# Performance work log

Hardware: AMD Instinct MI355X
Metric: run time of the kernel (lower is better)

The kernel has to match this reference:

```python
import jax, jax.numpy as jnp
import numpy as np

T, H, NH, NKV, HD, E, K, I = 1024, 2048, 16, 4, 128, 16, 2, 768
EPS = 1e-6
THETA = 10000.0


def setup_inputs() -> dict:
    key = jax.random.key(0)
    ks = jax.random.split(key, 8)
    s = 0.02
    return {
        "hidden_states": jax.random.normal(ks[0], (T, H), jnp.float32),
        "positions": jnp.arange(T, dtype=jnp.int32),
        "w_norm1": jnp.ones((H,), jnp.float32),
        "w_norm2": jnp.ones((H,), jnp.float32),
        "w_qkv": jax.random.normal(ks[1], (H, (NH + 2 * NKV) * HD), jnp.float32) * s,
        "w_qnorm": jnp.ones((HD,), jnp.float32),
        "w_knorm": jnp.ones((HD,), jnp.float32),
        "w_o": jax.random.normal(ks[2], (NH * HD, H), jnp.float32) * s,
        "w_router": jax.random.normal(ks[3], (H, E), jnp.float32) * s,
        "w_gate": jax.random.normal(ks[4], (E, H, I), jnp.float32) * s,
        "w_up": jax.random.normal(ks[5], (E, H, I), jnp.float32) * s,
        "w_down": jax.random.normal(ks[6], (E, I, H), jnp.float32) * s,
    }


def rmsnorm(x, w):
    return x * jax.lax.rsqrt(jnp.mean(x * x, axis=-1, keepdims=True) + EPS) * w


def apply_rope(x, positions):
    # NEOX-style rotary, full head_dim. x: [T, n_heads, HD]
    half = HD // 2
    inv_freq = 1.0 / (THETA ** (jnp.arange(half, dtype=jnp.float32) / half))
    ang = positions.astype(jnp.float32)[:, None] * inv_freq  # [T, half]
    cos = jnp.cos(ang)[:, None, :]
    sin = jnp.sin(ang)[:, None, :]
    x1, x2 = x[..., :half], x[..., half:]
    return jnp.concatenate([x1 * cos - x2 * sin, x2 * cos + x1 * sin], axis=-1)


def reference(hidden_states, positions, w_norm1, w_norm2, w_qkv, w_qnorm, w_knorm,
              w_o, w_router, w_gate, w_up, w_down):
    # prepare_attn: residual = x; h = input_layernorm(x)
    residual = hidden_states
    h = rmsnorm(hidden_states, w_norm1)

    # --- attention (bidirectional, GQA, per-head q/k RMSNorm + RoPE) ---
    qkv = h @ w_qkv
    q, k, v = jnp.split(qkv, [NH * HD, NH * HD + NKV * HD], axis=-1)
    q = rmsnorm(q.reshape(T, NH, HD), w_qnorm)
    k = rmsnorm(k.reshape(T, NKV, HD), w_knorm)
    v = v.reshape(T, NKV, HD)
    q = apply_rope(q, positions)
    k = apply_rope(k, positions)
    rep = NH // NKV
    kf = jnp.repeat(k, rep, axis=1)  # [T, NH, HD]
    vf = jnp.repeat(v, rep, axis=1)
    scores = jnp.einsum('tnd,snd->nts', q, kf) * (HD ** -0.5)  # [NH, T, T]
    p = jax.nn.softmax(scores, axis=-1)
    ctx = jnp.einsum('nts,snd->tnd', p, vf).reshape(T, NH * HD)
    attn_out = ctx @ w_o

    # prepare_mlp: residual = residual + attn_out; h = post_attention_layernorm(residual)
    residual = residual + attn_out
    h = rmsnorm(residual, w_norm2)

    # --- sparse MoE: softmax router, top-k renormalize, SwiGLU experts ---
    logits = h @ w_router
    probs = jax.nn.softmax(logits, axis=-1)
    topw, topi = jax.lax.top_k(probs, K)
    topw = topw / jnp.sum(topw, axis=-1, keepdims=True)
    gates = jnp.zeros((T, E), h.dtype).at[jnp.arange(T)[:, None], topi].set(topw)
    g = jnp.einsum('th,ehi->eti', h, w_gate)
    u = jnp.einsum('th,ehi->eti', h, w_up)
    y = jnp.einsum('eti,eih->eth', jax.nn.silu(g) * u, w_down)
    moe_out = jnp.einsum('eth,te->th', y, gates)

    return moe_out, residual
```

## Files before the change

### kernel.cpp

```cpp
#include <hip/hip_runtime.h>

#define T_    1024
#define H_    2048
#define NH_   16
#define NKV_  4
#define HD_   128
#define E_    16
#define I_    768
#define QKVN  3072

typedef __attribute__((ext_vector_type(8))) short  short8;
typedef __attribute__((ext_vector_type(4))) float  f32x4;
typedef unsigned short u16;

#define LDPA 32
#define LDPB 40

__device__ inline u16 f2bf(float f) {
  unsigned u = __builtin_bit_cast(unsigned, f);
  return (u16)((u + 0x7fffu + ((u >> 16) & 1u)) >> 16);
}
__device__ inline float bf2f(u16 h) {
  unsigned u = ((unsigned)h) << 16;
  return __builtin_bit_cast(float, u);
}

__device__ inline void gll16(const u16* g, u16* l) {
  __builtin_amdgcn_global_load_lds(
      (const __attribute__((address_space(1))) void*)g,
      (__attribute__((address_space(3))) void*)l, 16, 0, 0);
}

__device__ inline float blk_sum(float v, float* lds) {
#pragma unroll
  for (int o = 32; o; o >>= 1) v += __shfl_down(v, o);
  int w = threadIdx.x >> 6;
  __syncthreads();
  if ((threadIdx.x & 63) == 0) lds[w] = v;
  __syncthreads();
  float s = lds[0];
  int nw = blockDim.x >> 6;
  for (int i = 1; i < nw; ++i) s += lds[i];
  return s;
}
__device__ inline float blk_max(float v, float* lds) {
#pragma unroll
  for (int o = 32; o; o >>= 1) v = fmaxf(v, __shfl_down(v, o));
  int w = threadIdx.x >> 6;
  __syncthreads();
  if ((threadIdx.x & 63) == 0) lds[w] = v;
  __syncthreads();
  float s = lds[0];
  int nw = blockDim.x >> 6;
  for (int i = 1; i < nw; ++i) s = fmaxf(s, lds[i]);
  return s;
}


struct F4 { float v[4]; };

__device__ inline void wrS(u16* lds, const F4& r) {
  int n = threadIdx.x & 63, kh = (threadIdx.x >> 6) * 4;
  uint2 w;
  w.x = (unsigned)f2bf(r.v[0]) | ((unsigned)f2bf(r.v[1]) << 16);
  w.y = (unsigned)f2bf(r.v[2]) | ((unsigned)f2bf(r.v[3]) << 16);
  *(uint2*)(lds + n * LDPB + kh) = w;
}

template<int SA, int SB>
__device__ inline void mma2(const u16* As, const u16* Bs, f32x4 acc[2][2]) {
  const int lane = threadIdx.x & 63, wv = threadIdx.x >> 6;
  const int wr = wv >> 1, wc = wv & 1;
  const int kk = (lane >> 4) * 8, rr = lane & 15;
  short8 aF[2], bF[2];
#pragma unroll
  for (int m = 0; m < 2; ++m)
    aF[m] = *(const short8*)(As + (wr * 32 + m * 16 + rr) * SA + kk);
#pragma unroll
  for (int n = 0; n < 2; ++n)
    bF[n] = *(const short8*)(Bs + (wc * 32 + n * 16 + rr) * SB + kk);
#pragma unroll
  for (int m = 0; m < 2; ++m)
#pragma unroll
    for (int n = 0; n < 2; ++n)
      acc[m][n] = __builtin_amdgcn_mfma_f32_16x16x32_bf16(aF[m], bF[n], acc[m][n], 0, 0, 0);
}

#define ZERO_ACC(acc) do { \
  _Pragma("unroll") for (int m_ = 0; m_ < 2; ++m_) \
  _Pragma("unroll") for (int n_ = 0; n_ < 2; ++n_) acc[m_][n_] = (f32x4){0.f,0.f,0.f,0.f}; \
} while (0)

#define EPI_ROW(m, r)  (((threadIdx.x >> 6) >> 1) * 32 + (m)*16 + (((threadIdx.x&63) >> 4) * 4) + (r))
#define EPI_COL(n)     ((((threadIdx.x >> 6) & 1) * 32) + (n)*16 + ((threadIdx.x&63) & 15))

template<int NT, class GA, class LB>
__device__ inline void pipeGF(GA ga, LB lb, u16* A0, u16* B0, u16* A1, u16* B1,
                              f32x4 acc[2][2]) {
  F4 b0, b1;
  ga(A0, 0);
  lb(b0, 0); lb(b1, 1);
  wrS(B0, b0);
  if (NT > 2) lb(b0, 2);
#pragma unroll 1
  for (int kt = 0; kt < NT; kt += 2) {
    __syncthreads();
    ga(A1, kt + 1);
    wrS(B1, b1);
    if (kt + 3 < NT) lb(b1, kt + 3);
    mma2<LDPA, LDPB>(A0, B0, acc);
    __syncthreads();
    if (kt + 2 < NT) { ga(A0, kt + 2); wrS(B0, b0); }
    if (kt + 4 < NT) lb(b0, kt + 4);
    mma2<LDPA, LDPB>(A1, B1, acc);
  }
}

template<int NT, class GA, class GB>
__device__ inline void pipeGG(GA ga, GB gb, u16* A0, u16* B0, u16* A1, u16* B1,
                              f32x4 acc[2][2]) {
  ga(A0, 0); gb(B0, 0);
#pragma unroll 1
  for (int kt = 0; kt < NT; kt += 2) {
    __syncthreads();
    ga(A1, kt + 1); gb(B1, kt + 1);
    mma2<LDPA, LDPA>(A0, B0, acc);
    __syncthreads();
    if (kt + 2 < NT) { ga(A0, kt + 2); gb(B0, kt + 2); }
    mma2<LDPA, LDPA>(A1, B1, acc);
  }
}


__global__ __launch_bounds__(256) void k_rms1(const float* x, const float* w, u16* out) {
  __shared__ float lds[4];
  int t = blockIdx.x, tid = threadIdx.x;
  float v[8]; float ss = 0.f;
#pragma unroll
  for (int i = 0; i < 8; ++i) { v[i] = x[(size_t)t * H_ + tid + 256 * i]; ss += v[i] * v[i]; }
  ss = blk_sum(ss, lds);
  float inv = rsqrtf(ss * (1.f / H_) + 1e-6f);
#pragma unroll
  for (int i = 0; i < 8; ++i)
    out[(size_t)t * H_ + tid + 256 * i] = f2bf(v[i] * inv * w[tid + 256 * i]);
}

__global__ __launch_bounds__(256) void k_rms2(const float* x, const float* w,
                                              float* outf, u16* outb) {
  __shared__ float lds[4];
  int t = blockIdx.x, tid = threadIdx.x;
  float v[8]; float ss = 0.f;
#pragma unroll
  for (int i = 0; i < 8; ++i) { v[i] = x[(size_t)t * H_ + tid + 256 * i]; ss += v[i] * v[i]; }
  ss = blk_sum(ss, lds);
  float inv = rsqrtf(ss * (1.f / H_) + 1e-6f);
#pragma unroll
  for (int i = 0; i < 8; ++i) {
    float r = v[i] * inv * w[tid + 256 * i];
    outf[(size_t)t * H_ + tid + 256 * i] = r;
    outb[(size_t)t * H_ + tid + 256 * i] = f2bf(r);
  }
}

__global__ __launch_bounds__(512) void k_qkv(const u16* h1, const float* wqkv, float* qkv) {
  __shared__ __align__(16) u16 A0[128 * LDPA], A1[128 * LDPA];
  __shared__ __align__(16) u16 B0[64 * LDPB], B1[64 * LDPB];
  int bn = blockIdx.x, bm = blockIdx.y;
  f32x4 acc[2][2]; ZERO_ACC(acc);
  auto ga = [&](u16* As, int kt) {
    gll16(h1 + (size_t)(bm * 128 + (threadIdx.x >> 2)) * H_ + kt * 32 + (threadIdx.x & 3) * 8,
          As + (threadIdx.x & 448) * 8);
  };
  auto lb = [&](F4& r, int kt) {
    int n = threadIdx.x & 63, kh = (threadIdx.x >> 6) * 4;
    const float* src = wqkv + (size_t)(kt * 32 + kh) * QKVN + bn * 64 + n;
#pragma unroll
    for (int j = 0; j < 4; ++j) r.v[j] = src[(size_t)j * QKVN];
  };
  pipeGF<H_ / 32>(ga, lb, A0, B0, A1, B1, acc);
#pragma unroll
  for (int m = 0; m < 2; ++m)
#pragma unroll
    for (int n = 0; n < 2; ++n) {
      f32x4 a = acc[m][n];
#pragma unroll
      for (int r = 0; r < 4; ++r)
        qkv[(size_t)(bm * 128 + EPI_ROW(m, r)) * QKVN + bn * 64 + EPI_COL(n)] = a[r];
    }
}

__global__ __launch_bounds__(256) void k_qkrope(const float* qkv, const int* pos,
                                                const float* wq, const float* wk,
                                                u16* q, u16* kk, u16* vT) {
  __shared__ float cs[64], sn[64];
  int t = blockIdx.x, tid = threadIdx.x, lane = tid & 63, w = tid >> 6;
  if (tid < 64) {
    float fr = expf(-((float)tid / 64.f) * 9.210340371976184f);
    float ang = (float)pos[t] * fr;
    float s_, c_; sincosf(ang, &s_, &c_);
    cs[tid] = c_; sn[tid] = s_;
  }
  __syncthreads();
  const float* row = qkv + (size_t)t * QKVN;
  for (int h = w; h < NH_; h += 4) {
    float x1 = row[h * 128 + lane], x2 = row[h * 128 + 64 + lane];
    float ss = x1 * x1 + x2 * x2;
#pragma unroll
    for (int o = 32; o; o >>= 1) ss += __shfl_down(ss, o);
    ss = __shfl(ss, 0);
    float inv = rsqrtf(ss * (1.f / HD_) + 1e-6f);
    float n1 = x1 * inv * wq[lane], n2 = x2 * inv * wq[64 + lane];
    float o1 = n1 * cs[lane] - n2 * sn[lane];
    float o2 = n2 * cs[lane] + n1 * sn[lane];
    q[(size_t)t * (NH_ * HD_) + h * 128 + lane] = f2bf(o1);
    q[(size_t)t * (NH_ * HD_) + h * 128 + 64 + lane] = f2bf(o2);
  }
  if (w < NKV_) {
    int h = w;
    float x1 = row[2048 + h * 128 + lane], x2 = row[2048 + h * 128 + 64 + lane];
    float ss = x1 * x1 + x2 * x2;
#pragma unroll
    for (int o = 32; o; o >>= 1) ss += __shfl_down(ss, o);
    ss = __shfl(ss, 0);
    float inv = rsqrtf(ss * (1.f / HD_) + 1e-6f);
    float n1 = x1 * inv * wk[lane], n2 = x2 * inv * wk[64 + lane];
    float o1 = n1 * cs[lane] - n2 * sn[lane];
    float o2 = n2 * cs[lane] + n1 * sn[lane];
    kk[((size_t)h * T_ + t) * HD_ + lane] = f2bf(o1);
    kk[((size_t)h * T_ + t) * HD_ + 64 + lane] = f2bf(o2);
    float v1 = row[2560 + h * 128 + lane], v2 = row[2560 + h * 128 + 64 + lane];
    vT[((size_t)(h * 128 + lane)) * T_ + t] = f2bf(v1);
    vT[((size_t)(h * 128 + 64 + lane)) * T_ + t] = f2bf(v2);
  }
}

__global__ __launch_bounds__(512) void k_scores(const u16* q, const u16* kb, u16* S) {
  __shared__ __align__(16) u16 A0[128 * LDPA], A1[128 * LDPA];
  __shared__ __align__(16) u16 B0[64 * LDPA], B1[64 * LDPA];
  int h = blockIdx.x, sn = blockIdx.y, qm = blockIdx.z;
  const u16* Aq = q + h * 128;
  const u16* Bk = kb + (size_t)(h >> 2) * T_ * HD_;
  f32x4 acc[2][2]; ZERO_ACC(acc);
  auto ga = [&](u16* As, int kt) {
    gll16(Aq + (size_t)(qm * 128 + (threadIdx.x >> 2)) * (NH_ * HD_) + kt * 32 + (threadIdx.x & 3) * 8,
          As + (threadIdx.x & 448) * 8);
  };
  auto gb = [&](u16* Bs, int kt) {
    if (threadIdx.x < 256)
      gll16(Bk + (size_t)(sn * 64 + (threadIdx.x >> 2)) * HD_ + kt * 32 + (threadIdx.x & 3) * 8,
            Bs + (threadIdx.x & 192) * 8);
  };
  pipeGG<HD_ / 32>(ga, gb, A0, B0, A1, B1, acc);
  const float scale = 0.08838834764831845f;
#pragma unroll
  for (int m = 0; m < 2; ++m)
#pragma unroll
    for (int n = 0; n < 2; ++n) {
      f32x4 a = acc[m][n];
#pragma unroll
      for (int r = 0; r < 4; ++r)
        S[((size_t)h * T_ + qm * 128 + EPI_ROW(m, r)) * T_ + sn * 64 + EPI_COL(n)] =
            f2bf(a[r] * scale);
    }
}

__global__ __launch_bounds__(256) void k_softmax(u16* S) {
  __shared__ float lds[4];
  int t = blockIdx.x, h = blockIdx.y, tid = threadIdx.x;
  u16* rowp = S + ((size_t)h * T_ + t) * T_;
  float x[4];
#pragma unroll
  for (int i = 0; i < 4; ++i) x[i] = bf2f(rowp[tid + 256 * i]);
  float m = fmaxf(fmaxf(x[0], x[1]), fmaxf(x[2], x[3]));
  m = blk_max(m, lds);
  float s = 0.f;
#pragma unroll
  for (int i = 0; i < 4; ++i) { x[i] = __expf(x[i] - m); s += x[i]; }
  s = blk_sum(s, lds);
  float inv = 1.f / s;
#pragma unroll
  for (int i = 0; i < 4; ++i) rowp[tid + 256 * i] = f2bf(x[i] * inv);
}

__global__ __launch_bounds__(512) void k_pv(const u16* P, const u16* vT, u16* ctx) {
  __shared__ __align__(16) u16 A0[128 * LDPA], A1[128 * LDPA];
  __shared__ __align__(16) u16 B0[64 * LDPA], B1[64 * LDPA];
  int h = blockIdx.x, qm = blockIdx.y, nb = blockIdx.z;
  const u16* Ap = P + (size_t)h * T_ * T_;
  const u16* Bv = vT + (size_t)(h >> 2) * HD_ * T_ + (size_t)nb * 64 * T_;
  f32x4 acc[2][2]; ZERO_ACC(acc);
  auto ga = [&](u16* As, int kt) {
    gll16(Ap + (size_t)(qm * 128 + (threadIdx.x >> 2)) * T_ + kt * 32 + (threadIdx.x & 3) * 8,
          As + (threadIdx.x & 448) * 8);
  };
  auto gb = [&](u16* Bs, int kt) {
    if (threadIdx.x < 256)
      gll16(Bv + (size_t)(threadIdx.x >> 2) * T_ + kt * 32 + (threadIdx.x & 3) * 8,
            Bs + (threadIdx.x & 192) * 8);
  };
  pipeGG<T_ / 32>(ga, gb, A0, B0, A1, B1, acc);
#pragma unroll
  for (int m = 0; m < 2; ++m)
#pragma unroll
    for (int n = 0; n < 2; ++n) {
      f32x4 a = acc[m][n];
#pragma unroll
      for (int r = 0; r < 4; ++r)
        ctx[(size_t)(qm * 128 + EPI_ROW(m, r)) * (NH_ * HD_) + h * 128 + nb * 64 + EPI_COL(n)] =
            f2bf(a[r]);
    }
}

__global__ __launch_bounds__(512) void k_wo(const u16* ctx, const float* wo,
                                            const float* hs, float* resid) {
  __shared__ __align__(16) u16 A0[128 * LDPA], A1[128 * LDPA];
  __shared__ __align__(16) u16 B0[64 * LDPB], B1[64 * LDPB];
  int bn = blockIdx.x, bm = blockIdx.y;
  f32x4 acc[2][2]; ZERO_ACC(acc);
  auto ga = [&](u16* As, int kt) {
    gll16(ctx + (size_t)(bm * 128 + (threadIdx.x >> 2)) * H_ + kt * 32 + (threadIdx.x & 3) * 8,
          As + (threadIdx.x & 448) * 8);
  };
  auto lb = [&](F4& r, int kt) {
    int n = threadIdx.x & 63, kh = (threadIdx.x >> 6) * 4;
    const float* src = wo + (size_t)(kt * 32 + kh) * H_ + bn * 64 + n;
#pragma unroll
    for (int j = 0; j < 4; ++j) r.v[j] = src[(size_t)j * H_];
  };
  pipeGF<H_ / 32>(ga, lb, A0, B0, A1, B1, acc);
#pragma unroll
  for (int m = 0; m < 2; ++m)
#pragma unroll
    for (int n = 0; n < 2; ++n) {
      f32x4 a = acc[m][n];
#pragma unroll
      for (int r = 0; r < 4; ++r) {
        size_t idx = (size_t)(bm * 128 + EPI_ROW(m, r)) * H_ + bn * 64 + EPI_COL(n);
        resid[idx] = a[r] + hs[idx];
      }
    }
}

__global__ __launch_bounds__(256) void k_router(const float* h2f, const float* wr_,
                                                int* topi, float* topw, int* cnt) {
  __shared__ float xs[H_];
  __shared__ float red[4][16];
  __shared__ float lg[16];
  int t = blockIdx.x, tid = threadIdx.x;
#pragma unroll
  for (int i = 0; i < 8; ++i) xs[tid + 256 * i] = h2f[(size_t)t * H_ + tid + 256 * i];
  __syncthreads();
  int e = tid & 15, p = tid >> 4;
  float s = 0.f;
  int b0 = p * 128;
  for (int i = 0; i < 128; ++i) s += xs[b0 + i] * wr_[(size_t)(b0 + i) * E_ + e];
  s += __shfl_down(s, 32);
  s += __shfl_down(s, 16);
  int lane = tid & 63, w = tid >> 6;
  if (lane < 16) red[w][lane] = s;
  __syncthreads();
  if (tid < 16) lg[tid] = red[0][tid] + red[1][tid] + red[2][tid] + red[3][tid];
  __syncthreads();
  if (tid == 0) {
    float l1 = -1e30f; int e1 = 0;
    for (int i = 0; i < E_; ++i) if (lg[i] > l1) { l1 = lg[i]; e1 = i; }
    float l2 = -1e30f; int e2 = 0;
    for (int i = 0; i < E_; ++i) if (i != e1 && lg[i] > l2) { l2 = lg[i]; e2 = i; }
    float d = __expf(l2 - l1);
    float w1 = 1.f / (1.f + d), w2 = d / (1.f + d);
    topi[2 * t] = e1; topi[2 * t + 1] = e2;
    topw[2 * t] = w1; topw[2 * t + 1] = w2;
    atomicAdd(&cnt[e1], 1);
    atomicAdd(&cnt[e2], 1);
  }
}

__global__ void k_scan(const int* cnt, int* basearr) {
  if (threadIdx.x == 0) {
    int b = 0;
    for (int e = 0; e < E_; ++e) { basearr[e] = b; b += cnt[e]; }
    basearr[E_] = b;
  }
}

__global__ __launch_bounds__(256) void k_assign(const int* topi, const float* topw,
                                                const int* basearr, int* posc,
                                                int* tok, float* wslot) {
  int t = blockIdx.x * 256 + threadIdx.x;
  if (t < T_) {
#pragma unroll
    for (int j = 0; j < 2; ++j) {
      int e = topi[2 * t + j];
      int p = atomicAdd(&posc[e], 1);
      int s = basearr[e] + p;
      tok[s] = t;
      wslot[s] = topw[2 * t + j];
    }
  }
}

__global__ __launch_bounds__(512) void k_gateup(const u16* h2b,
                                                const float* wg, const float* wu,
                                                const int* cnt, const int* basearr, const int* tok,
                                                u16* act) {
  __shared__ __align__(16) u16 A0[128 * LDPA], A1[128 * LDPA];
  __shared__ __align__(16) u16 B0[64 * LDPB], B1[64 * LDPB];
  __shared__ int gat_s[128];
  int e = blockIdx.x;
  int c = cnt[e];
  int mt = blockIdx.z;
  if (mt * 128 >= c) return;
  int basee = basearr[e];
  int gmax = c - mt * 128;
  int n0 = blockIdx.y * 32;
  int tid = threadIdx.x;
  if (tid < 128) {
    int r = mt * 128 + tid;
    gat_s[tid] = (r < c) ? tok[basee + r] : tok[basee];
  }
  __syncthreads();
  int grow = gat_s[tid >> 2];
  const float* Bg = wg + (size_t)e * H_ * I_;
  const float* Bu = wu + (size_t)e * H_ * I_;
  f32x4 acc[2][2]; ZERO_ACC(acc);
  auto ga = [&](u16* As, int kt) {
    gll16(h2b + (size_t)grow * H_ + kt * 32 + (tid & 3) * 8, As + (tid & 448) * 8);
  };
  auto lb = [&](F4& r, int kt) {
    int cidx = tid & 63, kh = (tid >> 6) * 4;
    int fn = cidx >> 4;
    const float* base = (fn & 1) ? Bu : Bg;
    int col = n0 + (fn >> 1) * 16 + (cidx & 15);
    const float* src = base + (size_t)(kt * 32 + kh) * I_ + col;
#pragma unroll
    for (int j = 0; j < 4; ++j) r.v[j] = src[(size_t)j * I_];
  };
  pipeGF<H_ / 32>(ga, lb, A0, B0, A1, B1, acc);
  int slot0 = basee + mt * 128;
  int col = n0 + ((tid >> 6) & 1) * 16 + ((tid & 63) & 15);
#pragma unroll
  for (int m = 0; m < 2; ++m) {
#pragma unroll
    for (int r = 0; r < 4; ++r) {
      int row = EPI_ROW(m, r);
      if (row >= gmax) continue;
      float g = acc[m][0][r], u = acc[m][1][r];
      float sg = g / (1.f + __expf(-g));
      act[(size_t)(slot0 + row) * I_ + col] = f2bf(sg * u);
    }
  }
}

__global__ __launch_bounds__(512) void k_down(const u16* act, const float* wd,
                                              const int* cnt, const int* basearr,
                                              const int* tok, const float* wslot,
                                              float* moe) {
  __shared__ __align__(16) u16 A0[128 * LDPA], A1[128 * LDPA];
  __shared__ __align__(16) u16 B0[64 * LDPB], B1[64 * LDPB];
  int e = blockIdx.y;
  int c = cnt[e];
  int mt = blockIdx.z;
  if (mt * 128 >= c) return;
  int basee = basearr[e];
  int gmax = c - mt * 128;
  int slot0 = basee + mt * 128;
  int n0 = blockIdx.x * 64;
  const u16* Ap = act + (size_t)slot0 * I_;
  const float* Bp = wd + (size_t)e * I_ * H_;
  f32x4 acc[2][2]; ZERO_ACC(acc);
  auto ga = [&](u16* As, int kt) {
    gll16(Ap + (size_t)(threadIdx.x >> 2) * I_ + kt * 32 + (threadIdx.x & 3) * 8,
          As + (threadIdx.x & 448) * 8);
  };
  auto lb = [&](F4& r, int kt) {
    int n = threadIdx.x & 63, kh = (threadIdx.x >> 6) * 4;
    const float* src = Bp + (size_t)(kt * 32 + kh) * H_ + n0 + n;
#pragma unroll
    for (int j = 0; j < 4; ++j) r.v[j] = src[(size_t)j * H_];
  };
  pipeGF<I_ / 32>(ga, lb, A0, B0, A1, B1, acc);
#pragma unroll
  for (int m = 0; m < 2; ++m)
#pragma unroll
    for (int n = 0; n < 2; ++n) {
      f32x4 a = acc[m][n];
#pragma unroll
      for (int r = 0; r < 4; ++r) {
        int row = EPI_ROW(m, r);
        if (row >= gmax) continue;
        int col = EPI_COL(n);
        int slot = slot0 + row;
        float wgt = wslot[slot];
        int tk = tok[slot];
        atomicAdd(&moe[(size_t)tk * H_ + n0 + col], a[r] * wgt);
      }
    }
}

extern "C" void kernel_launch(void* const* d_in, const int* in_sizes, int n_in,
                              void* d_out, int out_size, void* d_ws, size_t ws_size,
                              hipStream_t stream) {
  const float* hs    = (const float*)d_in[0];
  const int*   pos   = (const int*)d_in[1];
  const float* wn1   = (const float*)d_in[2];
  const float* wn2   = (const float*)d_in[3];
  const float* wqkv  = (const float*)d_in[4];
  const float* wqn   = (const float*)d_in[5];
  const float* wkn   = (const float*)d_in[6];
  const float* wo    = (const float*)d_in[7];
  const float* wrt   = (const float*)d_in[8];
  const float* wg    = (const float*)d_in[9];
  const float* wu    = (const float*)d_in[10];
  const float* wd    = (const float*)d_in[11];
  float* out = (float*)d_out;
  float* moe_out = out;
  float* resid   = out + (size_t)T_ * H_;

  char* ws = (char*)d_ws;
  size_t off = 0;
  auto alloc = [&](size_t bytes) { size_t r = off; off = (off + bytes + 255) & ~(size_t)255; return r; };
  u16*   h1   = (u16*)  (ws + alloc((size_t)T_ * H_ * 2));
  float* qkv  = (float*)(ws + alloc((size_t)T_ * QKVN * 4));
  u16*   q    = (u16*)  (ws + alloc((size_t)T_ * NH_ * HD_ * 2));
  u16*   kb   = (u16*)  (ws + alloc((size_t)NKV_ * T_ * HD_ * 2));
  u16*   vT   = (u16*)  (ws + alloc((size_t)NKV_ * HD_ * T_ * 2));
  u16*   S    = (u16*)  (ws + alloc((size_t)NH_ * T_ * T_ * 2));
  u16*   ctx  = (u16*)  (ws + alloc((size_t)T_ * NH_ * HD_ * 2));
  float* h2f  = (float*)(ws + alloc((size_t)T_ * H_ * 4));
  u16*   h2b  = (u16*)  (ws + alloc((size_t)T_ * H_ * 2));
  u16*   act  = (u16*)  (ws + alloc((size_t)(2 * T_ + 256) * I_ * 2));
  int*   topi = (int*)  (ws + alloc((size_t)T_ * 2 * 4));
  float* topw = (float*)(ws + alloc((size_t)T_ * 2 * 4));
  int*   cnt  = (int*)  (ws + alloc(32 * 4));
  int*   posc = cnt + 16;
  int*   base = (int*)  (ws + alloc(32 * 4));
  int*   tok  = (int*)  (ws + alloc((size_t)(2 * T_ + 128) * 4));
  float* wsl  = (float*)(ws + alloc((size_t)(2 * T_ + 128) * 4));
  (void)ws_size; (void)in_sizes; (void)n_in; (void)out_size;

  hipMemsetAsync(moe_out, 0, (size_t)T_ * H_ * 4, stream);
  hipMemsetAsync(cnt, 0, 32 * 4, stream);

  k_rms1<<<T_, 256, 0, stream>>>(hs, wn1, h1);
  k_qkv<<<dim3(QKVN / 64, T_ / 128), 512, 0, stream>>>(h1, wqkv, qkv);
  k_qkrope<<<T_, 256, 0, stream>>>(qkv, pos, wqn, wkn, q, kb, vT);
  k_scores<<<dim3(NH_, T_ / 64, T_ / 128), 512, 0, stream>>>(q, kb, S);
  k_softmax<<<dim3(T_, NH_), 256, 0, stream>>>(S);
  k_pv<<<dim3(NH_, T_ / 128, HD_ / 64), 512, 0, stream>>>(S, vT, ctx);
  k_wo<<<dim3(H_ / 64, T_ / 128), 512, 0, stream>>>(ctx, wo, hs, resid);
  k_rms2<<<T_, 256, 0, stream>>>(resid, wn2, h2f, h2b);
  k_router<<<T_, 256, 0, stream>>>(h2f, wrt, topi, topw, cnt);
  k_scan<<<1, 64, 0, stream>>>(cnt, base);
  k_assign<<<4, 256, 0, stream>>>(topi, topw, base, posc, tok, wsl);
  k_gateup<<<dim3(E_, I_ / 32, T_ / 128), 512, 0, stream>>>(h2b, wg, wu, cnt, base, tok, act);
  k_down<<<dim3(H_ / 64, E_, T_ / 128), 512, 0, stream>>>(act, wd, cnt, base, tok, wsl, moe_out);
}
```

Measured before the change: 331.9 us.

## Fuse attention scores, softmax and PV into one flash-style kernel

Replaces the three separate kernels (QK^T scores to a global bf16 S matrix, row softmax, then P·V) with a single kernel. Each wave keeps a 16-row Q fragment in registers, streams 64-key K/V tiles through LDS, exponentiates the scores, stages P in LDS for the PV MFMA, and normalises by the row sum at the end. This removes the round trips of the 32 MB score matrix through global memory, plus two launches. The softmax skips max-subtraction, which is safe only because the q/k RMSNorm keeps the scaled scores bounded. Staging is single-buffered with no load/compute overlap, and the grid is only 256 blocks.

```diff
diff --git a/kernel.cpp b/kernel.cpp
--- a/kernel.cpp
+++ b/kernel.cpp
@@ -41,18 +41,6 @@
   float s = lds[0];
   int nw = blockDim.x >> 6;
   for (int i = 1; i < nw; ++i) s += lds[i];
-  return s;
-}
-__device__ inline float blk_max(float v, float* lds) {
-#pragma unroll
-  for (int o = 32; o; o >>= 1) v = fmaxf(v, __shfl_down(v, o));
-  int w = threadIdx.x >> 6;
-  __syncthreads();
-  if ((threadIdx.x & 63) == 0) lds[w] = v;
-  __syncthreads();
-  float s = lds[0];
-  int nw = blockDim.x >> 6;
-  for (int i = 1; i < nw; ++i) s = fmaxf(s, lds[i]);
   return s;
 }
 
@@ -116,21 +104,6 @@
   }
 }
 
-template<int NT, class GA, class GB>
-__device__ inline void pipeGG(GA ga, GB gb, u16* A0, u16* B0, u16* A1, u16* B1,
-                              f32x4 acc[2][2]) {
-  ga(A0, 0); gb(B0, 0);
-#pragma unroll 1
-  for (int kt = 0; kt < NT; kt += 2) {
-    __syncthreads();
-    ga(A1, kt + 1); gb(B1, kt + 1);
-    mma2<LDPA, LDPA>(A0, B0, acc);
-    __syncthreads();
-    if (kt + 2 < NT) { ga(A0, kt + 2); gb(B0, kt + 2); }
-    mma2<LDPA, LDPA>(A1, B1, acc);
-  }
-}
-
 
 __global__ __launch_bounds__(256) void k_rms1(const float* x, const float* w, u16* out) {
   __shared__ float lds[4];
@@ -234,81 +207,84 @@
   }
 }
 
-__global__ __launch_bounds__(512) void k_scores(const u16* q, const u16* kb, u16* S) {
-  __shared__ __align__(16) u16 A0[128 * LDPA], A1[128 * LDPA];
-  __shared__ __align__(16) u16 B0[64 * LDPA], B1[64 * LDPA];
-  int h = blockIdx.x, sn = blockIdx.y, qm = blockIdx.z;
-  const u16* Aq = q + h * 128;
-  const u16* Bk = kb + (size_t)(h >> 2) * T_ * HD_;
-  f32x4 acc[2][2]; ZERO_ACC(acc);
-  auto ga = [&](u16* As, int kt) {
-    gll16(Aq + (size_t)(qm * 128 + (threadIdx.x >> 2)) * (NH_ * HD_) + kt * 32 + (threadIdx.x & 3) * 8,
-          As + (threadIdx.x & 448) * 8);
-  };
-  auto gb = [&](u16* Bs, int kt) {
-    if (threadIdx.x < 256)
-      gll16(Bk + (size_t)(sn * 64 + (threadIdx.x >> 2)) * HD_ + kt * 32 + (threadIdx.x & 3) * 8,
-            Bs + (threadIdx.x & 192) * 8);
-  };
-  pipeGG<HD_ / 32>(ga, gb, A0, B0, A1, B1, acc);
+__global__ __launch_bounds__(256, 1) void k_fattn(const u16* q, const u16* kb,
+                                                  const u16* vT, u16* ctx) {
+  __shared__ __align__(16) u16 Ks[64 * 136];
+  __shared__ __align__(16) u16 Vs[128 * 72];
+  __shared__ __align__(16) u16 Ps[4 * 16 * 72];
+  int h = blockIdx.x, qt = blockIdx.y;
+  int tid = threadIdx.x, lane = tid & 63, wv = tid >> 6;
+  int rr = lane & 15, kk = (lane >> 4) * 8;
+  const u16* kbh = kb + (size_t)(h >> 2) * T_ * HD_;
+  const u16* vTh = vT + (size_t)(h >> 2) * HD_ * T_;
+  int q0 = qt * 64 + wv * 16;
+  short8 qf[4];
+#pragma unroll
+  for (int ks = 0; ks < 4; ++ks)
+    qf[ks] = *(const short8*)(q + (size_t)(q0 + rr) * (NH_ * HD_) + h * 128 + ks * 32 + kk);
+  f32x4 oacc[8];
+#pragma unroll
+  for (int i = 0; i < 8; ++i) oacc[i] = (f32x4){0.f, 0.f, 0.f, 0.f};
+  float lsum[4] = {0.f, 0.f, 0.f, 0.f};
   const float scale = 0.08838834764831845f;
-#pragma unroll
-  for (int m = 0; m < 2; ++m)
-#pragma unroll
-    for (int n = 0; n < 2; ++n) {
-      f32x4 a = acc[m][n];
-#pragma unroll
-      for (int r = 0; r < 4; ++r)
-        S[((size_t)h * T_ + qm * 128 + EPI_ROW(m, r)) * T_ + sn * 64 + EPI_COL(n)] =
-            f2bf(a[r] * scale);
-    }
-}
-
-__global__ __launch_bounds__(256) void k_softmax(u16* S) {
-  __shared__ float lds[4];
-  int t = blockIdx.x, h = blockIdx.y, tid = threadIdx.x;
-  u16* rowp = S + ((size_t)h * T_ + t) * T_;
-  float x[4];
-#pragma unroll
-  for (int i = 0; i < 4; ++i) x[i] = bf2f(rowp[tid + 256 * i]);
-  float m = fmaxf(fmaxf(x[0], x[1]), fmaxf(x[2], x[3]));
-  m = blk_max(m, lds);
-  float s = 0.f;
-#pragma unroll
-  for (int i = 0; i < 4; ++i) { x[i] = __expf(x[i] - m); s += x[i]; }
-  s = blk_sum(s, lds);
-  float inv = 1.f / s;
-#pragma unroll
-  for (int i = 0; i < 4; ++i) rowp[tid + 256 * i] = f2bf(x[i] * inv);
-}
-
-__global__ __launch_bounds__(512) void k_pv(const u16* P, const u16* vT, u16* ctx) {
-  __shared__ __align__(16) u16 A0[128 * LDPA], A1[128 * LDPA];
-  __shared__ __align__(16) u16 B0[64 * LDPA], B1[64 * LDPA];
-  int h = blockIdx.x, qm = blockIdx.y, nb = blockIdx.z;
-  const u16* Ap = P + (size_t)h * T_ * T_;
-  const u16* Bv = vT + (size_t)(h >> 2) * HD_ * T_ + (size_t)nb * 64 * T_;
-  f32x4 acc[2][2]; ZERO_ACC(acc);
-  auto ga = [&](u16* As, int kt) {
-    gll16(Ap + (size_t)(qm * 128 + (threadIdx.x >> 2)) * T_ + kt * 32 + (threadIdx.x & 3) * 8,
-          As + (threadIdx.x & 448) * 8);
-  };
-  auto gb = [&](u16* Bs, int kt) {
-    if (threadIdx.x < 256)
-      gll16(Bv + (size_t)(threadIdx.x >> 2) * T_ + kt * 32 + (threadIdx.x & 3) * 8,
-            Bs + (threadIdx.x & 192) * 8);
-  };
-  pipeGG<T_ / 32>(ga, gb, A0, B0, A1, B1, acc);
-#pragma unroll
-  for (int m = 0; m < 2; ++m)
-#pragma unroll
-    for (int n = 0; n < 2; ++n) {
-      f32x4 a = acc[m][n];
-#pragma unroll
-      for (int r = 0; r < 4; ++r)
-        ctx[(size_t)(qm * 128 + EPI_ROW(m, r)) * (NH_ * HD_) + h * 128 + nb * 64 + EPI_COL(n)] =
-            f2bf(a[r]);
-    }
+  u16* Pw = Ps + wv * 16 * 72;
+#pragma unroll 1
+  for (int kv = 0; kv < T_ / 64; ++kv) {
+    uint4 kreg[4], vreg[4];
+#pragma unroll
+    for (int i = 0; i < 4; ++i) {
+      int c = tid + 256 * i;
+      kreg[i] = *(const uint4*)(kbh + (size_t)(kv * 64 + (c >> 4)) * HD_ + (c & 15) * 8);
+      vreg[i] = *(const uint4*)(vTh + (size_t)(c >> 3) * T_ + kv * 64 + (c & 7) * 8);
+    }
+    __syncthreads();
+#pragma unroll
+    for (int i = 0; i < 4; ++i) {
+      int c = tid + 256 * i;
+      *(uint4*)(Ks + (c >> 4) * 136 + (c & 15) * 8) = kreg[i];
+      *(uint4*)(Vs + (c >> 3) * 72 + (c & 7) * 8) = vreg[i];
+    }
+    __syncthreads();
+    f32x4 sacc[4];
+#pragma unroll
+    for (int nf = 0; nf < 4; ++nf) sacc[nf] = (f32x4){0.f, 0.f, 0.f, 0.f};
+#pragma unroll
+    for (int ks = 0; ks < 4; ++ks)
+#pragma unroll
+      for (int nf = 0; nf < 4; ++nf) {
+        short8 bF = *(const short8*)(Ks + (nf * 16 + rr) * 136 + ks * 32 + kk);
+        sacc[nf] = __builtin_amdgcn_mfma_f32_16x16x32_bf16(qf[ks], bF, sacc[nf], 0, 0, 0);
+      }
+#pragma unroll
+    for (int nf = 0; nf < 4; ++nf)
+#pragma unroll
+      for (int r = 0; r < 4; ++r) {
+        float p = __expf(sacc[nf][r] * scale);
+        lsum[r] += p;
+        Pw[((lane >> 4) * 4 + r) * 72 + nf * 16 + rr] = f2bf(p);
+      }
+#pragma unroll
+    for (int ks2 = 0; ks2 < 2; ++ks2) {
+      short8 pa = *(const short8*)(Pw + rr * 72 + ks2 * 32 + kk);
+#pragma unroll
+      for (int nd = 0; nd < 8; ++nd) {
+        short8 bV = *(const short8*)(Vs + (nd * 16 + rr) * 72 + ks2 * 32 + kk);
+        oacc[nd] = __builtin_amdgcn_mfma_f32_16x16x32_bf16(pa, bV, oacc[nd], 0, 0, 0);
+      }
+    }
+  }
+#pragma unroll
+  for (int r = 0; r < 4; ++r) {
+#pragma unroll
+    for (int o = 1; o < 16; o <<= 1) lsum[r] += __shfl_xor(lsum[r], o);
+    lsum[r] = 1.f / lsum[r];
+  }
+#pragma unroll
+  for (int nd = 0; nd < 8; ++nd)
+#pragma unroll
+    for (int r = 0; r < 4; ++r)
+      ctx[(size_t)(q0 + (lane >> 4) * 4 + r) * (NH_ * HD_) + h * 128 + nd * 16 + rr] =
+          f2bf(oacc[nd][r] * lsum[r]);
 }
 
 __global__ __launch_bounds__(512) void k_wo(const u16* ctx, const float* wo,
@@ -524,7 +500,6 @@
   u16*   q    = (u16*)  (ws + alloc((size_t)T_ * NH_ * HD_ * 2));
   u16*   kb   = (u16*)  (ws + alloc((size_t)NKV_ * T_ * HD_ * 2));
   u16*   vT   = (u16*)  (ws + alloc((size_t)NKV_ * HD_ * T_ * 2));
-  u16*   S    = (u16*)  (ws + alloc((size_t)NH_ * T_ * T_ * 2));
   u16*   ctx  = (u16*)  (ws + alloc((size_t)T_ * NH_ * HD_ * 2));
   float* h2f  = (float*)(ws + alloc((size_t)T_ * H_ * 4));
   u16*   h2b  = (u16*)  (ws + alloc((size_t)T_ * H_ * 2));
@@ -544,9 +519,7 @@
   k_rms1<<<T_, 256, 0, stream>>>(hs, wn1, h1);
   k_qkv<<<dim3(QKVN / 64, T_ / 128), 512, 0, stream>>>(h1, wqkv, qkv);
   k_qkrope<<<T_, 256, 0, stream>>>(qkv, pos, wqn, wkn, q, kb, vT);
-  k_scores<<<dim3(NH_, T_ / 64, T_ / 128), 512, 0, stream>>>(q, kb, S);
-  k_softmax<<<dim3(T_, NH_), 256, 0, stream>>>(S);
-  k_pv<<<dim3(NH_, T_ / 128, HD_ / 64), 512, 0, stream>>>(S, vT, ctx);
+  k_fattn<<<dim3(NH_, T_ / 64), 256, 0, stream>>>(q, kb, vT, ctx);
   k_wo<<<dim3(H_ / 64, T_ / 128), 512, 0, stream>>>(ctx, wo, hs, resid);
   k_rms2<<<T_, 256, 0, stream>>>(resid, wn2, h2f, h2b);
   k_router<<<T_, 256, 0, stream>>>(h2f, wrt, topi, topw, cnt);
```

Measured after the change: 366.1 us. 10.3% more time.
